# Kernel tuning notes

Hardware: AMD Instinct MI355X
Metric: run time of the kernel (lower is better)

## Reference

```python
import jax, jax.numpy as jnp
import numpy as np

D = 1024
NH = 16
DH = D // NH
B = 2
N = 2048
EPS = 1e-5


def setup_inputs() -> dict:
    key = jax.random.key(0)
    ks = jax.random.split(key, 12)
    s = 0.02
    return {
        "x": jax.random.normal(ks[0], (B, N, D), jnp.float32),
        "Wq": jax.random.normal(ks[1], (D, D), jnp.float32) * s,
        "Wk": jax.random.normal(ks[2], (D, D), jnp.float32) * s,
        "Wv": jax.random.normal(ks[3], (D, D), jnp.float32) * s,
        "Wo": jax.random.normal(ks[4], (D, D), jnp.float32) * s,
        "bo": jnp.zeros((D,), jnp.float32),
        "ln1_scale": jnp.ones((D,), jnp.float32),
        "ln1_shift": jnp.zeros((D,), jnp.float32),
        "ln2_scale": jnp.ones((D,), jnp.float32),
        "ln2_shift": jnp.zeros((D,), jnp.float32),
        "W1": jax.random.normal(ks[5], (4 * D, D), jnp.float32) * s,
        "b1": jnp.zeros((4 * D,), jnp.float32),
        "W2": jax.random.normal(ks[6], (D, 4 * D), jnp.float32) * s,
        "b2": jnp.zeros((D,), jnp.float32),
    }


def _layernorm(x, scale, shift):
    mean = jnp.mean(x, axis=-1, keepdims=True)
    var = jnp.mean(jnp.square(x - mean), axis=-1, keepdims=True)  # unbiased=False
    return scale * ((x - mean) / jnp.sqrt(var + EPS)) + shift


def _gelu(x):
    c = jnp.sqrt(jnp.asarray(2.0 / jnp.pi, x.dtype))
    return 0.5 * x * (1.0 + jnp.tanh(c * (x + 0.044715 * x * x * x)))


def reference(x, Wq, Wk, Wv, Wo, bo, ln1_scale, ln1_shift, ln2_scale, ln2_shift, W1, b1, W2, b2):
    Bx, Nx, d = x.shape
    # pre-MHA LN
    h = _layernorm(x, ln1_scale, ln1_shift)
    # projections (torch Linear: y = h @ W.T), no bias for Wq/Wk/Wv
    q = (h @ Wq.T).reshape(Bx, Nx, NH, DH).transpose(0, 2, 1, 3)  # [B,nh,N,dh]
    k = (h @ Wk.T).reshape(Bx, Nx, NH, DH).transpose(0, 2, 1, 3)
    v = (h @ Wv.T).reshape(Bx, Nx, NH, DH).transpose(0, 2, 1, 3)
    s = jnp.einsum("bhnd,bhmd->bhnm", q, k)  # [B,nh,N,N]
    causal = jnp.tril(jnp.ones((Nx, Nx), bool))
    s = jnp.where(causal, s, -jnp.inf)
    p = jax.nn.softmax(s / jnp.sqrt(jnp.asarray(DH, s.dtype)), axis=-1)
    pv = jnp.einsum("bhnm,bhmd->bhnd", p, v)
    pv = pv.transpose(0, 2, 1, 3).reshape(Bx, Nx, d)
    attn = pv @ Wo.T + bo
    x = x + attn  # residual (dropout is identity, dpo=0)
    # pre-FFN LN + FFN
    h = _layernorm(x, ln2_scale, ln2_shift)
    h = _gelu(h @ W1.T + b1)
    h = h @ W2.T + b2
    return x + h
```

## Files before the change

kernel.cpp:

```cpp
#include <hip/hip_runtime.h>
#include <hip/hip_bf16.h>
#include <math.h>

#define Dmod   1024
#define NHmod  16
#define DHmod  64
#define Bmod   2
#define Nmod   2048
#define Mrows  (Bmod * Nmod)
#define FF     (4 * Dmod)
#define EPSLN  1e-5f

typedef __attribute__((ext_vector_type(8))) short bf16x8;
typedef __attribute__((ext_vector_type(4))) float f32x4;
typedef unsigned short ushort_t;
typedef unsigned int uint_t;

#define MFMA16x16x32(a, b, c) __builtin_amdgcn_mfma_f32_16x16x32_bf16((a), (b), (c), 0, 0, 0)

#define AS1 __attribute__((address_space(1)))
#define AS3 __attribute__((address_space(3)))

__device__ __forceinline__ void gload_lds16(const ushort_t* g, ushort_t* l) {
    __builtin_amdgcn_global_load_lds((const AS1 uint_t*)(const void*)g,
                                     (AS3 uint_t*)(void*)l, 16, 0, 0);
}

__device__ __forceinline__ ushort_t f2bf(float f) {
    union { float f; uint_t u; } v; v.f = f;
    uint_t r = v.u + 0x7FFFu + ((v.u >> 16) & 1u);
    return (ushort_t)(r >> 16);
}

__global__ __launch_bounds__(256) void cvt_kernel(const float* __restrict__ Wq, const float* __restrict__ Wk,
                                                  const float* __restrict__ Wv, const float* __restrict__ Wo,
                                                  const float* __restrict__ W1, const float* __restrict__ W2,
                                                  ushort_t* __restrict__ qkv, ushort_t* __restrict__ wo,
                                                  ushort_t* __restrict__ w1, ushort_t* __restrict__ w2) {
    int u = blockIdx.x * 256 + threadIdx.x;
    const float* src; ushort_t* dst; int i;
    float scale = 1.0f;
    if (u < 393216) {
        if (u < 131072)      { src = Wq; dst = qkv;           i = u; scale = 0.125f; }
        else if (u < 262144) { src = Wk; dst = qkv + 1048576; i = u - 131072; }
        else                 { src = Wv; dst = qkv + 2097152; i = u - 262144; }
    } else if (u < 524288)   { src = Wo; dst = wo; i = u - 393216; }
    else if (u < 1048576)    { src = W1; dst = w1; i = u - 524288; }
    else                     { src = W2; dst = w2; i = u - 1048576; }
    float4 a = ((const float4*)src)[2 * i];
    float4 b = ((const float4*)src)[2 * i + 1];
    uint4 o;
    o.x = (uint_t)f2bf(a.x * scale) | ((uint_t)f2bf(a.y * scale) << 16);
    o.y = (uint_t)f2bf(a.z * scale) | ((uint_t)f2bf(a.w * scale) << 16);
    o.z = (uint_t)f2bf(b.x * scale) | ((uint_t)f2bf(b.y * scale) << 16);
    o.w = (uint_t)f2bf(b.z * scale) | ((uint_t)f2bf(b.w * scale) << 16);
    ((uint4*)dst)[i] = o;
}

__global__ __launch_bounds__(256) void ln_bf_kernel(const float* __restrict__ x,
                                                    const float* __restrict__ scale,
                                                    const float* __restrict__ shift,
                                                    ushort_t* __restrict__ out) {
    int row = blockIdx.x;
    const float4* xr = (const float4*)(x + (size_t)row * Dmod);
    float4 v = xr[threadIdx.x];
    float s  = v.x + v.y + v.z + v.w;
    float s2 = v.x*v.x + v.y*v.y + v.z*v.z + v.w*v.w;

    __shared__ float rs[8], rs2[8];
    #pragma unroll
    for (int o = 32; o; o >>= 1) { s += __shfl_down(s, o); s2 += __shfl_down(s2, o); }
    int wave = threadIdx.x >> 6, lane = threadIdx.x & 63;
    if (lane == 0) { rs[wave] = s; rs2[wave] = s2; }
    __syncthreads();
    if (threadIdx.x == 0) {
        rs[0]  = rs[0] + rs[1] + rs[2] + rs[3];
        rs2[0] = rs2[0] + rs2[1] + rs2[2] + rs2[3];
    }
    __syncthreads();
    float mean = rs[0] * (1.0f / Dmod);
    float var  = rs2[0] * (1.0f / Dmod) - mean * mean;
    float rstd = rsqrtf(var + EPSLN);

    float4 sc = ((const float4*)scale)[threadIdx.x];
    float4 sh = ((const float4*)shift)[threadIdx.x];
    uint2 o;
    o.x = (uint_t)f2bf(sc.x * (v.x - mean) * rstd + sh.x) |
          ((uint_t)f2bf(sc.y * (v.y - mean) * rstd + sh.y) << 16);
    o.y = (uint_t)f2bf(sc.z * (v.z - mean) * rstd + sh.z) |
          ((uint_t)f2bf(sc.w * (v.w - mean) * rstd + sh.w) << 16);
    ((uint2*)(out + (size_t)row * Dmod))[threadIdx.x] = o;
}

__device__ __forceinline__ float gelu_f(float x) {
    const float c = 0.7978845608028654f;
    float u = c * (x + 0.044715f * x * x * x);
    return x / (1.0f + __expf(-2.0f * u));
}

template <int MODE, int BN>
__global__ __launch_bounds__(256) void bgemm(const ushort_t* __restrict__ A,
                                             const ushort_t* __restrict__ W,
                                             const float* __restrict__ bias,
                                             const float* __restrict__ resid,
                                             void* __restrict__ Cv,
                                             int M, int Nout, int K, int KS,
                                             int GN, int GM) {
    const int BSZ = BN * 32;
    const int NFR = BN / 32;
    __shared__ ushort_t As[2 * 4096];
    __shared__ ushort_t Bs[2 * BSZ];
    int tid  = threadIdx.x;
    int w    = tid >> 6, lane = tid & 63;
    int li   = lane & 15, g = lane >> 4;
    int wr   = w >> 1,  wc = w & 1;

    int xcd = blockIdx.x & 7;
    int c   = blockIdx.x >> 3;
    int RN  = GN >> 2;
    int RM  = GM >> 1;
    int rsz = RN * RM;
    int bz  = c / rsz;
    int r   = c - bz * rsz;
    int bm  = (xcd >> 2) * RM + r / RN;
    int bn  = (xcd & 3) * RN + r % RN;

    int srow = tid >> 2;
    int scol = ((tid & 3) ^ ((tid >> 3) & 3)) * 8;
    const ushort_t* Ag = A + (size_t)(bm * 128 + srow) * K + bz * KS + scol;
    const ushort_t* Wg = W + (size_t)(bn * BN  + srow) * K + bz * KS + scol;
    ushort_t* AsW = As + w * 512;
    ushort_t* BsW = Bs + w * 512;

    int rsw = ((g ^ ((li >> 1) & 3)) * 8);

    f32x4 acc[4][NFR];
    #pragma unroll
    for (int i = 0; i < 4; i++)
        #pragma unroll
        for (int j = 0; j < NFR; j++) acc[i][j] = (f32x4){0.f, 0.f, 0.f, 0.f};

    const int NT = KS >> 5;

    gload_lds16(Ag,          AsW);
    gload_lds16(Ag + 64 * K, AsW + 2048);
    gload_lds16(Wg,          BsW);
    if (BN == 128) gload_lds16(Wg + 64 * K, BsW + 2048);
    __syncthreads();

    for (int t = 0; t < NT; ++t) {
        if (t + 1 < NT) {
            int k0 = (t + 1) * 32;
            int na = ((t + 1) & 1) * 4096;
            int nb = ((t + 1) & 1) * BSZ;
            gload_lds16(Ag + k0,          AsW + na);
            gload_lds16(Ag + 64 * K + k0, AsW + na + 2048);
            gload_lds16(Wg + k0,          BsW + nb);
            if (BN == 128) gload_lds16(Wg + 64 * K + k0, BsW + nb + 2048);
        }
        int ca = (t & 1) * 4096;
        int cb = (t & 1) * BSZ;
        bf16x8 af[4], bfr[NFR];
        #pragma unroll
        for (int mi = 0; mi < 4; mi++)
            af[mi] = *(const bf16x8*)&As[ca + (wr * 64 + mi * 16 + li) * 32 + rsw];
        #pragma unroll
        for (int ni = 0; ni < NFR; ni++)
            bfr[ni] = *(const bf16x8*)&Bs[cb + (wc * (BN / 2) + ni * 16 + li) * 32 + rsw];
        #pragma unroll
        for (int mi = 0; mi < 4; mi++)
            #pragma unroll
            for (int ni = 0; ni < NFR; ni++)
                acc[mi][ni] = MFMA16x16x32(af[mi], bfr[ni], acc[mi][ni]);
        __syncthreads();
    }

    #pragma unroll
    for (int mi = 0; mi < 4; mi++) {
        #pragma unroll
        for (int ni = 0; ni < NFR; ni++) {
            int nn = bn * BN + wc * (BN / 2) + ni * 16 + li;
            #pragma unroll
            for (int r2 = 0; r2 < 4; r2++) {
                int m = bm * 128 + wr * 64 + mi * 16 + g * 4 + r2;
                float v = acc[mi][ni][r2];
                if (MODE == 1) {
                    float* C = (float*)Cv;
                    C[(size_t)m * Nout + nn] = v + bias[nn] + resid[(size_t)m * Nout + nn];
                } else if (MODE == 2) {
                    ushort_t* C = (ushort_t*)Cv;
                    C[(size_t)m * Nout + nn] = f2bf(gelu_f(v + bias[nn]));
                } else if (MODE == 3) {
                    float* C = (float*)Cv + (size_t)bz * M * Nout;
                    C[(size_t)m * Nout + nn] = v;
                } else {
                    int which = nn >> 10;
                    int col   = nn & 1023;
                    int h = col >> 6, d = col & 63;
                    int b = m >> 11,  n = m & (Nmod - 1);
                    ushort_t* C = (ushort_t*)Cv;
                    if (which == 0)
                        C[(((size_t)(b * NHmod + h)) * Nmod + n) * DHmod + d] = f2bf(v);
                    else if (which == 1)
                        C[4194304u + (((size_t)(b * NHmod + h)) * Nmod + n) * DHmod + d] = f2bf(v);
                    else
                        C[8388608u + (((size_t)(b * NHmod + h)) * DHmod + d) * Nmod + n] = f2bf(v);
                }
            }
        }
    }
}

__global__ __launch_bounds__(256) void red_ln_kernel(const float* __restrict__ p,
                                                     const float* __restrict__ x,
                                                     const float* __restrict__ bo,
                                                     const float* __restrict__ scale,
                                                     const float* __restrict__ shift,
                                                     float* __restrict__ x1,
                                                     ushort_t* __restrict__ h2) {
    int row = blockIdx.x;
    int t   = threadIdx.x;
    const size_t MD = (size_t)Mrows * Dmod;
    float4 a = ((const float4*)(p + (size_t)row * Dmod))[t];
    float4 b = ((const float4*)(p + MD + (size_t)row * Dmod))[t];
    float4 xr = ((const float4*)(x + (size_t)row * Dmod))[t];
    float4 bb = ((const float4*)bo)[t];
    float4 v;
    v.x = a.x + b.x + xr.x + bb.x;
    v.y = a.y + b.y + xr.y + bb.y;
    v.z = a.z + b.z + xr.z + bb.z;
    v.w = a.w + b.w + xr.w + bb.w;
    ((float4*)(x1 + (size_t)row * Dmod))[t] = v;

    float s  = v.x + v.y + v.z + v.w;
    float s2 = v.x*v.x + v.y*v.y + v.z*v.z + v.w*v.w;
    __shared__ float rs[8], rs2[8];
    #pragma unroll
    for (int o = 32; o; o >>= 1) { s += __shfl_down(s, o); s2 += __shfl_down(s2, o); }
    int wave = t >> 6, lane = t & 63;
    if (lane == 0) { rs[wave] = s; rs2[wave] = s2; }
    __syncthreads();
    if (t == 0) {
        rs[0]  = rs[0] + rs[1] + rs[2] + rs[3];
        rs2[0] = rs2[0] + rs2[1] + rs2[2] + rs2[3];
    }
    __syncthreads();
    float mean = rs[0] * (1.0f / Dmod);
    float var  = rs2[0] * (1.0f / Dmod) - mean * mean;
    float rstd = rsqrtf(var + EPSLN);

    float4 sc = ((const float4*)scale)[t];
    float4 sh = ((const float4*)shift)[t];
    uint2 o;
    o.x = (uint_t)f2bf(sc.x * (v.x - mean) * rstd + sh.x) |
          ((uint_t)f2bf(sc.y * (v.y - mean) * rstd + sh.y) << 16);
    o.y = (uint_t)f2bf(sc.z * (v.z - mean) * rstd + sh.z) |
          ((uint_t)f2bf(sc.w * (v.w - mean) * rstd + sh.w) << 16);
    ((uint2*)(h2 + (size_t)row * Dmod))[t] = o;
}

__global__ __launch_bounds__(256) void red_out_kernel(const float* __restrict__ p,
                                                      const float* __restrict__ x1,
                                                      const float* __restrict__ b2,
                                                      float* __restrict__ out) {
    const size_t MD4 = (size_t)Mrows * Dmod / 4;
    size_t i = (size_t)blockIdx.x * 256 + threadIdx.x;
    if (i >= MD4) return;
    float4 a = ((const float4*)p)[i];
    float4 b = ((const float4*)p)[MD4 + i];
    float4 xr = ((const float4*)x1)[i];
    float4 bb = ((const float4*)b2)[i & 255];
    float4 v;
    v.x = a.x + b.x + xr.x + bb.x;
    v.y = a.y + b.y + xr.y + bb.y;
    v.z = a.z + b.z + xr.z + bb.z;
    v.w = a.w + b.w + xr.w + bb.w;
    ((float4*)out)[i] = v;
}

__global__ __launch_bounds__(256) void fattn_kernel(const ushort_t* __restrict__ Q,
                                                    const ushort_t* __restrict__ K,
                                                    const ushort_t* __restrict__ VT,
                                                    ushort_t* __restrict__ O) {
    int bid = blockIdx.x;
    int xcd = bid & 7;
    int j   = bid >> 3;
    int bh  = xcd * 4 + (j & 3);
    int qt  = 31 - (j >> 2);
    int b   = bh >> 4, hh = bh & 15;
    int w    = threadIdx.x >> 6;
    int lane = threadIdx.x & 63;
    int li   = lane & 15;
    int g    = lane >> 4;

    __shared__ ushort_t Klds[2][4096];
    __shared__ ushort_t Vlds[2][4096];
    __shared__ ushort_t Plds[4][16][72];

    int q0 = qt * 64 + w * 16;
    int q  = q0 + li;

    const ushort_t* Qb = Q  + (size_t)bh * Nmod * DHmod;
    const ushort_t* Kb = K  + (size_t)bh * Nmod * DHmod;
    const ushort_t* Vb = VT + (size_t)bh * DHmod * Nmod;

    bf16x8 qf[2];
    #pragma unroll
    for (int c = 0; c < 2; c++)
        qf[c] = *(const bf16x8*)(Qb + (size_t)q * DHmod + c * 32 + g * 8);

    f32x4 po[4];
    #pragma unroll
    for (int mt = 0; mt < 4; mt++) po[mt] = (f32x4){0.f, 0.f, 0.f, 0.f};
    float l = 0.f;

    const int ntiles = qt + 1;

    int r_sub = lane >> 3;
    int cc    = ((lane & 7) ^ (r_sub & 7)) * 8;

    int swz  = (li & 7) * 8;
    int roff = li * 64;
    int c0k  = (g * 8) ^ swz;
    int c1k  = (32 + g * 8) ^ swz;

    auto stage = [&](int buf, int kt) {
        int k0 = kt * 64;
        #pragma unroll
        for (int i2 = 0; i2 < 2; i2++) {
            int i   = w * 2 + i2;
            int row = i * 8 + r_sub;
            gload_lds16(Kb + (size_t)(k0 + row) * DHmod + cc, &Klds[buf][i * 512]);
            gload_lds16(Vb + (size_t)row * Nmod + k0 + cc,    &Vlds[buf][i * 512]);
        }
    };

    stage(0, 0);

    for (int kt = 0; kt < ntiles; ++kt) {
        __syncthreads();
        if (kt + 1 < ntiles) stage((kt + 1) & 1, kt + 1);
        int cur = kt & 1;
        int k0  = kt * 64;

        f32x4 s[4];
        __builtin_amdgcn_s_setprio(1);
        #pragma unroll
        for (int mt = 0; mt < 4; mt++) {
            bf16x8 kf0 = *(const bf16x8*)&Klds[cur][mt * 1024 + roff + c0k];
            bf16x8 kf1 = *(const bf16x8*)&Klds[cur][mt * 1024 + roff + c1k];
            s[mt] = (f32x4){0.f, 0.f, 0.f, 0.f};
            s[mt] = MFMA16x16x32(kf0, qf[0], s[mt]);
            s[mt] = MFMA16x16x32(kf1, qf[1], s[mt]);
        }
        __builtin_amdgcn_s_setprio(0);

        if (kt == qt) {
            #pragma unroll
            for (int mt = 0; mt < 4; mt++)
                #pragma unroll
                for (int r = 0; r < 4; r++)
                    if (k0 + mt * 16 + g * 4 + r > q) s[mt][r] = -INFINITY;
        }
        float ptile = 0.f;
        #pragma unroll
        for (int mt = 0; mt < 4; mt++) {
            float p0 = __expf(s[mt][0]);
            float p1 = __expf(s[mt][1]);
            float p2 = __expf(s[mt][2]);
            float p3 = __expf(s[mt][3]);
            ptile += (p0 + p1) + (p2 + p3);
            uint2 pk;
            pk.x = (uint_t)f2bf(p0) | ((uint_t)f2bf(p1) << 16);
            pk.y = (uint_t)f2bf(p2) | ((uint_t)f2bf(p3) << 16);
            *(uint2*)&Plds[w][li][mt * 16 + g * 4] = pk;
        }
        l += ptile;

        asm volatile("" ::: "memory");

        bf16x8 pf0 = *(const bf16x8*)&Plds[w][li][g * 8];
        bf16x8 pf1 = *(const bf16x8*)&Plds[w][li][32 + g * 8];
        __builtin_amdgcn_s_setprio(1);
        #pragma unroll
        for (int mt = 0; mt < 4; mt++) {
            bf16x8 vf0 = *(const bf16x8*)&Vlds[cur][mt * 1024 + roff + c0k];
            bf16x8 vf1 = *(const bf16x8*)&Vlds[cur][mt * 1024 + roff + c1k];
            po[mt] = MFMA16x16x32(vf0, pf0, po[mt]);
            po[mt] = MFMA16x16x32(vf1, pf1, po[mt]);
        }
        __builtin_amdgcn_s_setprio(0);
        asm volatile("" ::: "memory");
    }

    l += __shfl_xor(l, 16);
    l += __shfl_xor(l, 32);
    float inv = 1.0f / l;
    ushort_t* Orow = O + ((size_t)(b * Nmod + q)) * Dmod + hh * DHmod;
    #pragma unroll
    for (int mt = 0; mt < 4; mt++) {
        uint2 pk;
        pk.x = (uint_t)f2bf(po[mt][0] * inv) | ((uint_t)f2bf(po[mt][1] * inv) << 16);
        pk.y = (uint_t)f2bf(po[mt][2] * inv) | ((uint_t)f2bf(po[mt][3] * inv) << 16);
        *(uint2*)(Orow + mt * 16 + g * 4) = pk;
    }
}

extern "C" void kernel_launch(void* const* d_in, const int* in_sizes, int n_in,
                              void* d_out, int out_size, void* d_ws, size_t ws_size,
                              hipStream_t stream) {
    const float* x    = (const float*)d_in[0];
    const float* Wq   = (const float*)d_in[1];
    const float* Wk   = (const float*)d_in[2];
    const float* Wv   = (const float*)d_in[3];
    const float* Wo   = (const float*)d_in[4];
    const float* bo   = (const float*)d_in[5];
    const float* ln1s = (const float*)d_in[6];
    const float* ln1b = (const float*)d_in[7];
    const float* ln2s = (const float*)d_in[8];
    const float* ln2b = (const float*)d_in[9];
    const float* W1   = (const float*)d_in[10];
    const float* b1   = (const float*)d_in[11];
    const float* W2   = (const float*)d_in[12];
    const float* b2   = (const float*)d_in[13];
    float* out = (float*)d_out;
    char*  wsb = (char*)d_ws;

    ushort_t* h_bf  = (ushort_t*)wsb;
    ushort_t* qb    = (ushort_t*)(wsb + (8u  << 20));
    ushort_t* kb    = qb + 4194304;
    ushort_t* vtb   = qb + 8388608;
    float*    x1    = (float*)(wsb + (32u << 20));
    ushort_t* h2_bf = (ushort_t*)(wsb + (48u << 20));
    ushort_t* g_bf  = (ushort_t*)(wsb + (56u << 20));
    ushort_t* wqkv  = (ushort_t*)(wsb + (88u << 20));
    ushort_t* wo_b  = (ushort_t*)(wsb + (94u << 20));
    ushort_t* w1_b  = (ushort_t*)(wsb + (96u << 20));
    ushort_t* w2_b  = (ushort_t*)(wsb + (104u << 20));
    ushort_t* att   = h_bf;
    float* pWo = (float*)(wsb + (56u << 20));
    float* pFd = (float*)wsb;

    cvt_kernel<<<6144, 256, 0, stream>>>(Wq, Wk, Wv, Wo, W1, W2, wqkv, wo_b, w1_b, w2_b);
    ln_bf_kernel<<<Mrows, 256, 0, stream>>>(x, ln1s, ln1b, h_bf);
    bgemm<0, 128><<<768, 256, 0, stream>>>(h_bf, wqkv, nullptr, nullptr, qb, Mrows, 3072, Dmod, Dmod, 24, 32);
    fattn_kernel<<<1024, 256, 0, stream>>>(qb, kb, vtb, att);
    bgemm<3, 64><<<1024, 256, 0, stream>>>(att, wo_b, nullptr, nullptr, pWo, Mrows, Dmod, Dmod, Dmod / 2, 16, 32);
    red_ln_kernel<<<Mrows, 256, 0, stream>>>(pWo, x, bo, ln2s, ln2b, x1, h2_bf);
    bgemm<2, 128><<<1024, 256, 0, stream>>>(h2_bf, w1_b, b1, nullptr, g_bf, Mrows, FF, Dmod, Dmod, 32, 32);
    bgemm<3, 64><<<1024, 256, 0, stream>>>(g_bf, w2_b, nullptr, nullptr, pFd, Mrows, Dmod, FF, FF / 2, 16, 32);
    red_out_kernel<<<(Mrows * Dmod / 4 + 255) / 256, 256, 0, stream>>>(pFd, x1, b2, out);
}
```

Measured before the change: 260.2 us.

## Triple-buffer GEMM LDS staging with one barrier per K-step and inline-asm reads

Moves the bf16 GEMM mainloop from double to triple-buffered LDS staging. Tiles are prefetched two steps ahead, and partial vmcnt waits plus a single s_barrier per iteration replace the trailing __syncthreads. LDS fragment reads become hand-written ds_read_b128 with immediate offsets, and the MFMA block is wrapped in s_setprio. The goal is to hide global-load latency and cut barrier stalls. The cost is more LDS per block, which may lower occupancy, and fragile manual waitcnt accounting.

```diff
diff --git a/kernel.cpp b/kernel.cpp
--- a/kernel.cpp
+++ b/kernel.cpp
@@ -108,8 +108,8 @@
                                              int GN, int GM) {
     const int BSZ = BN * 32;
     const int NFR = BN / 32;
-    __shared__ ushort_t As[2 * 4096];
-    __shared__ ushort_t Bs[2 * BSZ];
+    __shared__ ushort_t As[3 * 4096];
+    __shared__ ushort_t Bs[3 * BSZ];
     int tid  = threadIdx.x;
     int w    = tid >> 6, lane = tid & 63;
     int li   = lane & 15, g = lane >> 4;
@@ -134,6 +134,11 @@
 
     int rsw = ((g ^ ((li >> 1) & 3)) * 8);
 
+    uint_t lbA = (uint_t)(uintptr_t)(&As[0]);
+    uint_t lbB = (uint_t)(uintptr_t)(&Bs[0]);
+    uint_t abase = lbA + (uint_t)(((wr * 64 + li) * 32 + rsw) * 2);
+    uint_t bbase = lbB + (uint_t)(((wc * (BN / 2) + li) * 32 + rsw) * 2);
+
     f32x4 acc[4][NFR];
     #pragma unroll
     for (int i = 0; i < 4; i++)
@@ -142,37 +147,54 @@
 
     const int NT = KS >> 5;
 
-    gload_lds16(Ag,          AsW);
-    gload_lds16(Ag + 64 * K, AsW + 2048);
-    gload_lds16(Wg,          BsW);
-    if (BN == 128) gload_lds16(Wg + 64 * K, BsW + 2048);
-    __syncthreads();
+    auto stagef = [&](int bufA, int bufB, int t) {
+        int k0 = t * 32;
+        gload_lds16(Ag + k0,          AsW + bufA);
+        gload_lds16(Ag + 64 * K + k0, AsW + bufA + 2048);
+        gload_lds16(Wg + k0,          BsW + bufB);
+        if (BN == 128) gload_lds16(Wg + 64 * K + k0, BsW + bufB + 2048);
+    };
+
+    stagef(0, 0, 0);
+    stagef(4096, BSZ, 1);
+
+    int curA = 0, curB = 0;
+    int stgA = 8192, stgB = 2 * BSZ;
 
     for (int t = 0; t < NT; ++t) {
-        if (t + 1 < NT) {
-            int k0 = (t + 1) * 32;
-            int na = ((t + 1) & 1) * 4096;
-            int nb = ((t + 1) & 1) * BSZ;
-            gload_lds16(Ag + k0,          AsW + na);
-            gload_lds16(Ag + 64 * K + k0, AsW + na + 2048);
-            gload_lds16(Wg + k0,          BsW + nb);
-            if (BN == 128) gload_lds16(Wg + 64 * K + k0, BsW + nb + 2048);
-        }
-        int ca = (t & 1) * 4096;
-        int cb = (t & 1) * BSZ;
+        if (t == NT - 1) { asm volatile("s_waitcnt vmcnt(0)" ::); }
+        else if (BN == 128) { asm volatile("s_waitcnt vmcnt(4)" ::); }
+        else { asm volatile("s_waitcnt vmcnt(3)" ::); }
+        __builtin_amdgcn_s_barrier();
+        __builtin_amdgcn_sched_barrier(0);
+        if (t + 2 < NT) stagef(stgA, stgB, t + 2);
+        __builtin_amdgcn_sched_barrier(0);
         bf16x8 af[4], bfr[NFR];
-        #pragma unroll
-        for (int mi = 0; mi < 4; mi++)
-            af[mi] = *(const bf16x8*)&As[ca + (wr * 64 + mi * 16 + li) * 32 + rsw];
-        #pragma unroll
-        for (int ni = 0; ni < NFR; ni++)
-            bfr[ni] = *(const bf16x8*)&Bs[cb + (wc * (BN / 2) + ni * 16 + li) * 32 + rsw];
+        uint_t aa = abase + (uint_t)(curA * 2);
+        uint_t bb = bbase + (uint_t)(curB * 2);
+        asm volatile("ds_read_b128 %0, %1"             : "=v"(af[0]) : "v"(aa));
+        asm volatile("ds_read_b128 %0, %1 offset:1024" : "=v"(af[1]) : "v"(aa));
+        asm volatile("ds_read_b128 %0, %1 offset:2048" : "=v"(af[2]) : "v"(aa));
+        asm volatile("ds_read_b128 %0, %1 offset:3072" : "=v"(af[3]) : "v"(aa));
+        asm volatile("ds_read_b128 %0, %1"             : "=v"(bfr[0]) : "v"(bb));
+        asm volatile("ds_read_b128 %0, %1 offset:1024" : "=v"(bfr[1]) : "v"(bb));
+        if (NFR == 4) {
+            asm volatile("ds_read_b128 %0, %1 offset:2048" : "=v"(bfr[2]) : "v"(bb));
+            asm volatile("ds_read_b128 %0, %1 offset:3072" : "=v"(bfr[3]) : "v"(bb));
+        }
+        asm volatile("s_waitcnt lgkmcnt(0)" ::);
+        __builtin_amdgcn_sched_barrier(0);
+        __builtin_amdgcn_s_setprio(1);
         #pragma unroll
         for (int mi = 0; mi < 4; mi++)
             #pragma unroll
             for (int ni = 0; ni < NFR; ni++)
                 acc[mi][ni] = MFMA16x16x32(af[mi], bfr[ni], acc[mi][ni]);
-        __syncthreads();
+        __builtin_amdgcn_s_setprio(0);
+        curA = (curA == 8192) ? 0 : curA + 4096;
+        curB = (curB == 2 * BSZ) ? 0 : curB + BSZ;
+        stgA = (stgA == 8192) ? 0 : stgA + 4096;
+        stgB = (stgB == 2 * BSZ) ? 0 : stgB + BSZ;
     }
 
     #pragma unroll
```

Result: faster. 252.7 us (-2.9%).
